# Optimization experiments

Hardware: AMD Instinct MI355X
Metric: run time of the kernel (lower is better)

Reference implementation:

```python
import jax, jax.numpy as jnp
import numpy as np

DIM = 4096
N_HEADS = 32
N_KV_HEADS = 8
HEAD_DIM = DIM // N_HEADS      # 128
N_REP = N_HEADS // N_KV_HEADS  # 4
B, S = 2, 2048
THETA = 10000.0


def _rope_tables(seq_len, head_dim):
    # standard llama2.c freqs: [1, S, 1, head_dim//2]
    freqs = 1.0 / (THETA ** (np.arange(0, head_dim, 2, dtype=np.float32) / head_dim))
    t = np.arange(seq_len, dtype=np.float32)
    ang = np.outer(t, freqs)  # [S, head_dim//2]
    cos = jnp.asarray(np.cos(ang))[None, :, None, :]
    sin = jnp.asarray(np.sin(ang))[None, :, None, :]
    return cos, sin


def setup_inputs() -> dict:
    key = jax.random.key(0)
    ks = jax.random.split(key, 5)
    x = jax.random.normal(ks[0], (B, S, DIM), dtype=jnp.float32)
    freqs_cos, freqs_sin = _rope_tables(S, HEAD_DIM)
    scale = 1.0 / np.sqrt(DIM)
    wq = jax.random.normal(ks[1], (DIM, N_HEADS * HEAD_DIM), dtype=jnp.float32) * scale
    wk = jax.random.normal(ks[2], (DIM, N_KV_HEADS * HEAD_DIM), dtype=jnp.float32) * scale
    wv = jax.random.normal(ks[3], (DIM, N_KV_HEADS * HEAD_DIM), dtype=jnp.float32) * scale
    wo = jax.random.normal(ks[4], (N_HEADS * HEAD_DIM, DIM), dtype=jnp.float32) * scale
    return {"x": x, "freqs_cos": freqs_cos, "freqs_sin": freqs_sin,
            "wq": wq, "wk": wk, "wv": wv, "wo": wo}


def _apply_rotary(t, cos, sin):
    # t: [B, S, H, head_dim]; cos/sin: [1, S, 1, head_dim//2]
    b, s, h, d = t.shape
    tr = t.reshape(b, s, h, d // 2, 2)
    t_r, t_i = tr[..., 0], tr[..., 1]
    out_r = t_r * cos - t_i * sin
    out_i = t_r * sin + t_i * cos
    return jnp.stack([out_r, out_i], axis=-1).reshape(b, s, h, d)


def reference(x, freqs_cos, freqs_sin, wq, wk, wv, wo):
    b, s, _ = x.shape
    q = (x @ wq).reshape(b, s, N_HEADS, HEAD_DIM)
    k = (x @ wk).reshape(b, s, N_KV_HEADS, HEAD_DIM)
    v = (x @ wv).reshape(b, s, N_KV_HEADS, HEAD_DIM)
    q = _apply_rotary(q, freqs_cos, freqs_sin)
    k = _apply_rotary(k, freqs_cos, freqs_sin)
    # GQA: repeat kv heads to match q heads
    k = jnp.repeat(k, N_REP, axis=2)  # [b, s, H, hd]
    v = jnp.repeat(v, N_REP, axis=2)
    # NOTE: source calls SDPA with attn_mask=None and no is_causal -> non-causal
    scores = jnp.einsum('bqhd,bkhd->bhqk', q, k) / jnp.sqrt(
        jnp.asarray(HEAD_DIM, dtype=q.dtype))
    attn = jax.nn.softmax(scores, axis=-1)
    out = jnp.einsum('bhqk,bkhd->bqhd', attn, v)
    out = out.reshape(b, s, N_HEADS * HEAD_DIM)
    return out @ wo
```

## Files before the change

kernel.cpp:

```cpp
#include <hip/hip_runtime.h>
#include <cstdint>


typedef __attribute__((ext_vector_type(8))) short short8;
typedef __attribute__((ext_vector_type(4))) float f32x4;
typedef __attribute__((ext_vector_type(16))) float f32x16;

__device__ __forceinline__ float bf2f(unsigned short u) {
  union { unsigned int i; float f; } v; v.i = ((unsigned int)u) << 16; return v.f;
}
__device__ __forceinline__ unsigned short f2bf(float f) {
  union { float f; unsigned int i; } v; v.f = f;
  unsigned int r = v.i + 0x7fffu + ((v.i >> 16) & 1u);
  return (unsigned short)(r >> 16);
}

__device__ __forceinline__ void gload_lds16(const void* g, void* lds) {
  __builtin_amdgcn_global_load_lds(
      (const __attribute__((address_space(1))) unsigned int*)g,
      (__attribute__((address_space(3))) unsigned int*)lds, 16, 0, 0);
}

__device__ __forceinline__ unsigned int cvtpk_bf16(float lo, float hi) {
  unsigned int r;
  asm("v_cvt_pk_bf16_f32 %0, %1, %2" : "=v"(r) : "v"(lo), "v"(hi));
  return r;
}
__device__ __forceinline__ void pl32swap(unsigned int& a, unsigned int& b) {
  asm("v_permlane32_swap_b32 %0, %1" : "+v"(a), "+v"(b));
}


__global__ __launch_bounds__(256) void cast_bf16(const float* __restrict__ src,
                                                 unsigned short* __restrict__ dst) {
  size_t i = (size_t)blockIdx.x * 256 + threadIdx.x;
  float4 v = ((const float4*)src)[i];
  ushort4 o; o.x = f2bf(v.x); o.y = f2bf(v.y); o.z = f2bf(v.z); o.w = f2bf(v.w);
  ((ushort4*)dst)[i] = o;
}

__global__ __launch_bounds__(256) void transpose_cast(const float* __restrict__ src,
                                                      unsigned short* __restrict__ dst,
                                                      int R, int C) {
  __shared__ float tile[32][33];
  int c0 = blockIdx.x * 32, r0 = blockIdx.y * 32;
  int tx = threadIdx.x & 31, ty = threadIdx.x >> 5;
#pragma unroll
  for (int j = 0; j < 4; ++j)
    tile[ty + j * 8][tx] = src[(size_t)(r0 + ty + j * 8) * C + c0 + tx];
  __syncthreads();
#pragma unroll
  for (int j = 0; j < 4; ++j)
    dst[(size_t)(c0 + ty + j * 8) * R + r0 + tx] = f2bf(tile[tx][ty + j * 8]);
}

__global__ __launch_bounds__(256) void rope_k(unsigned short* __restrict__ qkv,
                                              const float* __restrict__ cosT,
                                              const float* __restrict__ sinT) {
  int idx = blockIdx.x * 256 + threadIdx.x;
  int t = idx / 640;
  int cb = (idx - t * 640) * 8;
  int s = t & 2047;
  int j0 = (cb & 127) >> 1;
  unsigned short* p = qkv + (size_t)t * 6144 + cb;
  uint4 u = *(const uint4*)p;
  float4 c4 = *(const float4*)&cosT[s * 64 + j0];
  float4 s4 = *(const float4*)&sinT[s * 64 + j0];
  auto rot = [](unsigned int& uu, float c, float sn) {
    float re = bf2f((unsigned short)(uu & 0xffffu));
    float im = bf2f((unsigned short)(uu >> 16));
    float nr = re * c - im * sn;
    float ni = re * sn + im * c;
    uu = (unsigned int)f2bf(nr) | ((unsigned int)f2bf(ni) << 16);
  };
  rot(u.x, c4.x, s4.x); rot(u.y, c4.y, s4.y);
  rot(u.z, c4.z, s4.z); rot(u.w, c4.w, s4.w);
  *(uint4*)p = u;
}

__global__ __launch_bounds__(256) void transpose_v(const unsigned short* __restrict__ qkv,
                                                   unsigned short* __restrict__ vt) {
  __shared__ unsigned short tile[32][33];
  int bk = blockIdx.z;
  int s0 = blockIdx.x * 32, d0 = blockIdx.y * 32;
  int tx = threadIdx.x & 31, ty = threadIdx.x >> 5;
  int b = bk >> 3, kvh = bk & 7;
#pragma unroll
  for (int j = 0; j < 4; ++j)
    tile[ty + j * 8][tx] =
        qkv[(size_t)(b * 2048 + s0 + ty + j * 8) * 6144 + 5120 + kvh * 128 + d0 + tx];
  __syncthreads();
#pragma unroll
  for (int j = 0; j < 4; ++j)
    vt[(size_t)(bk * 128 + d0 + ty + j * 8) * 2048 + s0 + tx] = tile[tx][ty + j * 8];
}


#define GBAR() asm volatile("s_barrier" ::: "memory")
#define GVM6() asm volatile("s_waitcnt vmcnt(6)" ::: "memory")
#define GVM4() asm volatile("s_waitcnt vmcnt(4)" ::: "memory")
#define GHINT() asm volatile("s_waitcnt lgkmcnt(8)" ::: "memory")

#define GLDA(buf, mh)                                                                   \
  do {                                                                                  \
    _Pragma("unroll") for (int m_ = 0; m_ < 4; ++m_)                                    \
    _Pragma("unroll") for (int ks_ = 0; ks_ < 2; ++ks_)                                 \
      a[m_][ks_] = *(const short8*)&smem[buf][0]                                        \
          [(wm * 128 + (mh) * 64 + m_ * 16 + lr) * 64 + (((ks_ * 4 + lg) ^ (lr & 7)) << 3)]; \
  } while (0)

#define GLDB(bf_, buf, nh)                                                              \
  do {                                                                                  \
    _Pragma("unroll") for (int n_ = 0; n_ < 2; ++n_)                                    \
    _Pragma("unroll") for (int ks_ = 0; ks_ < 2; ++ks_)                                 \
      bf_[n_][ks_] = *(const short8*)&smem[buf][1]                                      \
          [(wn * 64 + (nh) * 32 + n_ * 16 + lr) * 64 + (((ks_ * 4 + lg) ^ (lr & 7)) << 3)]; \
  } while (0)

#define GMM(bf_, mh, nh)                                                                \
  do {                                                                                  \
    __builtin_amdgcn_s_setprio(1);                                                      \
    _Pragma("unroll") for (int ks_ = 0; ks_ < 2; ++ks_)                                 \
    _Pragma("unroll") for (int m_ = 0; m_ < 4; ++m_)                                    \
    _Pragma("unroll") for (int n_ = 0; n_ < 2; ++n_)                                    \
      acc[(mh) * 4 + m_][(nh) * 2 + n_] = __builtin_amdgcn_mfma_f32_16x16x32_bf16(      \
          a[m_][ks_], bf_[n_][ks_], acc[(mh) * 4 + m_][(nh) * 2 + n_], 0, 0, 0);        \
    __builtin_amdgcn_s_setprio(0);                                                      \
  } while (0)

#define GSTG(half, buf, tile)                                                           \
  do {                                                                                  \
    _Pragma("unroll") for (int t2_ = 0; t2_ < 2; ++t2_)                                 \
      gload_lds16(srcp[half][t2_] + ((size_t)(tile) << 6),                              \
                  &smem[buf][(half) >> 1][dsto[half][t2_]]);                            \
  } while (0)

template <typename OutT>
__device__ __forceinline__ void gemm256_body(const unsigned short* __restrict__ A,
                                             const unsigned short* __restrict__ B,
                                             OutT* __restrict__ C, int K, int ldc,
                                             unsigned short (*smem)[2][16384]) {
  const int bid = blockIdx.x;
  const int xcd = bid & 7, ii = bid >> 3;
  const int mt = (xcd & 3) * 4 + (ii & 3);
  const int nt = (xcd >> 2) * 8 + (ii >> 2);
  const int m0 = mt * 256, n0 = nt * 256;
  const int tid = threadIdx.x, w = tid >> 6, l = tid & 63;
  const int wm = w >> 2, wn = w & 3;
  const int lr = l & 15, lg = l >> 4;
  const int NT = K >> 6;

  const int lsub = l >> 3, lgr = l & 7;
  const int sg = (lgr ^ lsub) << 3;
  const unsigned short* srcp[4][2];
  int dsto[4][2];
#pragma unroll
  for (int t2 = 0; t2 < 2; ++t2) {
    int lb = t2 * 64 + w * 8;
    int pa0 = (lb & 63) + ((lb >> 6) << 7);
    int pb0 = (lb & 31) + ((lb >> 5) << 6);
    srcp[0][t2] = A + (size_t)(m0 + pa0 + lsub) * K + sg;       dsto[0][t2] = pa0 * 64;
    srcp[1][t2] = A + (size_t)(m0 + pa0 + 64 + lsub) * K + sg;  dsto[1][t2] = (pa0 + 64) * 64;
    srcp[2][t2] = B + (size_t)(n0 + pb0 + lsub) * K + sg;       dsto[2][t2] = pb0 * 64;
    srcp[3][t2] = B + (size_t)(n0 + pb0 + 32 + lsub) * K + sg;  dsto[3][t2] = (pb0 + 32) * 64;
  }

  f32x4 acc[8][4] = {};
  short8 a[4][2], b0f[2][2], b1f[2][2];

  GSTG(0, 0, 0); GSTG(2, 0, 0); GSTG(3, 0, 0); GSTG(1, 0, 0);
  GSTG(0, 1, 1); GSTG(2, 1, 1); GSTG(3, 1, 1);
  GVM6();
  GBAR();

  for (int t = 0; t < NT / 2; ++t) {
    const int t1 = 2 * t + 1;
    const int t2a = (2 * t + 2 < NT) ? 2 * t + 2 : NT - 1;
    const int t2b = (2 * t + 3 < NT) ? 2 * t + 3 : NT - 1;
    GLDA(0, 0); GLDB(b0f, 0, 0);
    GSTG(1, 1, t1);
    GHINT();
    GBAR(); GMM(b0f, 0, 0); GBAR();
    GLDB(b1f, 0, 1);
    GSTG(0, 0, t2a);
    GBAR(); GMM(b1f, 0, 1); GBAR();
    GLDA(0, 1);
    GSTG(2, 0, t2a);
    GBAR(); GMM(b0f, 1, 0); GBAR();
    GSTG(3, 0, t2a);
    GBAR(); GMM(b1f, 1, 1); GVM6(); GBAR();
    GLDA(1, 0); GLDB(b0f, 1, 0);
    GSTG(1, 0, t2a);
    GHINT();
    GBAR(); GMM(b0f, 0, 0); GBAR();
    GLDB(b1f, 1, 1);
    GSTG(0, 1, t2b);
    GBAR(); GMM(b1f, 0, 1); GBAR();
    GLDA(1, 1);
    GSTG(2, 1, t2b);
    GBAR(); GMM(b0f, 1, 0); GBAR();
    GSTG(3, 1, t2b);
    GBAR(); GMM(b1f, 1, 1); GVM6(); GBAR();
  }

#pragma unroll
  for (int m = 0; m < 8; ++m)
#pragma unroll
    for (int n = 0; n < 4; ++n)
#pragma unroll
      for (int r = 0; r < 4; ++r) {
        int row = m0 + wm * 128 + m * 16 + lg * 4 + r;
        int col = n0 + wn * 64 + n * 16 + lr;
        float v = acc[m][n][r];
        if constexpr (sizeof(OutT) == 2)
          C[(size_t)row * ldc + col] = (OutT)f2bf(v);
        else
          C[(size_t)row * ldc + col] = v;
      }
}

__global__ __launch_bounds__(512) void gemm_qproj(const unsigned short* __restrict__ A,
                                                  const unsigned short* __restrict__ B,
                                                  unsigned short* __restrict__ C,
                                                  int K, int ldc) {
  __shared__ unsigned short smem[2][2][16384];
  gemm256_body<unsigned short>(A, B, C, K, ldc, smem);
}

__global__ __launch_bounds__(512) void gemm_oproj(const unsigned short* __restrict__ A,
                                                  const unsigned short* __restrict__ B,
                                                  float* __restrict__ C,
                                                  int K, int ldc) {
  __shared__ unsigned short smem[2][2][16384];
  gemm256_body<float>(A, B, C, K, ldc, smem);
}


#define KLDA(buf)                                                                       \
  do {                                                                                  \
    _Pragma("unroll") for (int m_ = 0; m_ < 4; ++m_)                                    \
    _Pragma("unroll") for (int ks_ = 0; ks_ < 2; ++ks_)                                 \
      a2[m_][ks_] = *(const short8*)&As2[buf]                                           \
          [(wm * 64 + m_ * 16 + lr) * 64 + (((ks_ * 4 + lg) ^ (lr & 7)) << 3)];         \
  } while (0)

#define KLDB(bf_, buf, nh)                                                              \
  do {                                                                                  \
    _Pragma("unroll") for (int n_ = 0; n_ < 2; ++n_)                                    \
    _Pragma("unroll") for (int ks_ = 0; ks_ < 2; ++ks_)                                 \
      bf_[n_][ks_] = *(const short8*)&Bs2[buf]                                          \
          [(wn * 64 + (nh) * 32 + n_ * 16 + lr) * 64 + (((ks_ * 4 + lg) ^ (lr & 7)) << 3)]; \
  } while (0)

#define KMM(bf_, nh)                                                                    \
  do {                                                                                  \
    __builtin_amdgcn_s_setprio(1);                                                      \
    _Pragma("unroll") for (int ks_ = 0; ks_ < 2; ++ks_)                                 \
    _Pragma("unroll") for (int m_ = 0; m_ < 4; ++m_)                                    \
    _Pragma("unroll") for (int n_ = 0; n_ < 2; ++n_)                                    \
      acc[m_][(nh) * 2 + n_] = __builtin_amdgcn_mfma_f32_16x16x32_bf16(                 \
          a2[m_][ks_], bf_[n_][ks_], acc[m_][(nh) * 2 + n_], 0, 0, 0);                  \
    __builtin_amdgcn_s_setprio(0);                                                      \
  } while (0)

#define KSTGA(buf, tile)                                                                \
  do {                                                                                  \
    _Pragma("unroll") for (int t2_ = 0; t2_ < 2; ++t2_)                                 \
      gload_lds16(srcA[t2_] + ((size_t)(tile) << 6), &As2[buf][dstA[t2_]]);             \
  } while (0)
#define KSTGB0(buf, tile)                                                               \
  do {                                                                                  \
    _Pragma("unroll") for (int t2_ = 0; t2_ < 2; ++t2_)                                 \
      gload_lds16(srcB0[t2_] + ((size_t)(tile) << 6), &Bs2[buf][dstB0[t2_]]);           \
  } while (0)
#define KSTGB1(buf, tile)                                                               \
  do {                                                                                  \
    _Pragma("unroll") for (int t2_ = 0; t2_ < 2; ++t2_)                                 \
      gload_lds16(srcB1[t2_] + ((size_t)(tile) << 6), &Bs2[buf][dstB1[t2_]]);           \
  } while (0)

__global__ __launch_bounds__(512) void gemm_kvproj(const unsigned short* __restrict__ A,
                                                   const unsigned short* __restrict__ B,
                                                   unsigned short* __restrict__ C,
                                                   int K, int ldc) {
  __shared__ unsigned short As2[2][8192];
  __shared__ unsigned short Bs2[2][16384];
  const int bid = blockIdx.x;
  const int xcd = bid & 7, ii = bid >> 3;
  const int mt = (xcd & 3) * 8 + (ii & 7);
  const int nt = (xcd >> 2) * 4 + (ii >> 3);
  const int m0 = mt * 128, n0 = nt * 256;
  const int tid = threadIdx.x, w = tid >> 6, l = tid & 63;
  const int wm = w >> 2, wn = w & 3;
  const int lr = l & 15, lg = l >> 4;
  const int NT = K >> 6;

  const int lsub = l >> 3, lgr = l & 7;
  const int sg = (lgr ^ lsub) << 3;
  const unsigned short* srcA[2];  int dstA[2];
  const unsigned short* srcB0[2]; int dstB0[2];
  const unsigned short* srcB1[2]; int dstB1[2];
#pragma unroll
  for (int t2 = 0; t2 < 2; ++t2) {
    int ra = t2 * 64 + w * 8;
    srcA[t2] = A + (size_t)(m0 + ra + lsub) * K + sg;            dstA[t2] = ra * 64;
    int lb = t2 * 64 + w * 8;
    int pb0 = (lb & 31) + ((lb >> 5) << 6);
    srcB0[t2] = B + (size_t)(n0 + pb0 + lsub) * K + sg;          dstB0[t2] = pb0 * 64;
    srcB1[t2] = B + (size_t)(n0 + pb0 + 32 + lsub) * K + sg;     dstB1[t2] = (pb0 + 32) * 64;
  }

  f32x4 acc[4][4] = {};
  short8 a2[4][2], bb0[2][2], bb1[2][2];

  KSTGA(0, 0); KSTGB0(0, 0); KSTGB1(0, 0);
  KSTGA(1, 1); KSTGB0(1, 1);
  GVM4();
  GBAR();

  for (int t = 0; t < NT / 2; ++t) {
    const int t1 = 2 * t + 1;
    const int t2a = (2 * t + 2 < NT) ? 2 * t + 2 : NT - 1;
    const int t2b = (2 * t + 3 < NT) ? 2 * t + 3 : NT - 1;
    KLDA(0); KLDB(bb0, 0, 0);
    KSTGB1(1, t1);
    GHINT();
    GBAR(); KMM(bb0, 0); GBAR();
    KLDB(bb1, 0, 1);
    KSTGA(0, t2a); KSTGB0(0, t2a);
    GBAR(); KMM(bb1, 1); GVM4(); GBAR();
    KLDA(1); KLDB(bb0, 1, 0);
    KSTGB1(0, t2a);
    GHINT();
    GBAR(); KMM(bb0, 0); GBAR();
    KLDB(bb1, 1, 1);
    KSTGA(1, t2b); KSTGB0(1, t2b);
    GBAR(); KMM(bb1, 1); GVM4(); GBAR();
  }

#pragma unroll
  for (int m = 0; m < 4; ++m)
#pragma unroll
    for (int n = 0; n < 4; ++n)
#pragma unroll
      for (int r = 0; r < 4; ++r) {
        int row = m0 + wm * 64 + m * 16 + lg * 4 + r;
        int col = n0 + wn * 64 + n * 16 + lr;
        C[(size_t)row * ldc + col] = f2bf(acc[m][n][r]);
      }
}


__global__ __launch_bounds__(256, 2) void attn_k(const unsigned short* __restrict__ qkv,
                                                 const unsigned short* __restrict__ vt,
                                                 unsigned short* __restrict__ ctx) {
  __shared__ unsigned short Ks[2][64 * 128];
  __shared__ unsigned short Vs[2][128 * 64];
  const int bid = blockIdx.x;
  const int xcd = bid & 7, idx = bid >> 3;
  const int kvg = xcd * 2 + (idx >> 6);
  const int hg = (idx >> 4) & 3;
  const int qt = idx & 15;
  const int b = kvg >> 3, kvh = kvg & 7, h = kvh * 4 + hg;
  const int w = threadIdx.x >> 6, l = threadIdx.x & 63;
  const int lc = l & 31, hi = l >> 5;
  const size_t tok0 = (size_t)b * 2048;
  const int q0 = qt * 128 + w * 32;
  const float C2 = 0.12751744516557944f;
  const float THR = 4.0f / C2;

  const unsigned short* ksrc[4];
  const unsigned short* vsrc[4];
#pragma unroll
  for (int i = 0; i < 4; ++i) {
    int L = w * 256 + i * 64 + l;
    int krow = L >> 4, kc = L & 15;
    ksrc[i] = qkv + (tok0 + krow) * 6144 + 4096 + kvh * 128 + ((kc ^ (krow & 7)) << 3);
    int vrow = L >> 3, vc = L & 7;
    vsrc[i] = vt + (size_t)(kvg * 128 + vrow) * 2048 + ((vc ^ (vrow & 7)) << 3);
  }
  const int ldsBase = (w * 256) * 8;

  auto stage = [&](int bufi, int kv0s) {
#pragma unroll
    for (int i = 0; i < 4; ++i)
      gload_lds16(ksrc[i] + (size_t)kv0s * 6144, &Ks[bufi][ldsBase + i * 512]);
#pragma unroll
    for (int i = 0; i < 4; ++i)
      gload_lds16(vsrc[i] + kv0s, &Vs[bufi][ldsBase + i * 512]);
  };

  const unsigned short* Qb = qkv + (tok0 + q0 + lc) * 6144 + h * 128 + hi * 8;
  short8 qf[8];
#pragma unroll
  for (int dc = 0; dc < 8; ++dc) qf[dc] = *(const short8*)(Qb + dc * 16);

  f32x16 acc[4] = {};
  float m = -1e30f, lsum = 0.f;

  stage(0, 0);
  __syncthreads();

  int buf = 0;
  for (int kt = 0; kt < 32; ++kt) {
    if (kt < 31) stage(buf ^ 1, (kt + 1) * 64);
    const int swz = (lc & 7) << 3;
    f32x16 s0 = {}, s1 = {};
#pragma unroll
    for (int dc = 0; dc < 8; ++dc) {
      int cidx = ((dc * 2 + hi) << 3) ^ swz;
      short8 kf0 = *(const short8*)&Ks[buf][lc * 128 + cidx];
      short8 kf1 = *(const short8*)&Ks[buf][(lc + 32) * 128 + cidx];
      s0 = __builtin_amdgcn_mfma_f32_32x32x16_bf16(kf0, qf[dc], s0, 0, 0, 0);
      s1 = __builtin_amdgcn_mfma_f32_32x32x16_bf16(kf1, qf[dc], s1, 0, 0, 0);
    }
    float tm = fmaxf(s0[0], s1[0]);
#pragma unroll
    for (int r = 1; r < 16; ++r) tm = fmaxf(tm, fmaxf(s0[r], s1[r]));
    tm = fmaxf(tm, __shfl_xor(tm, 32, 64));
    if (__any(tm > m + THR)) {
      float mn = fmaxf(m, tm);
      float sc = __builtin_amdgcn_exp2f((m - mn) * C2);
      m = mn;
      lsum *= sc;
#pragma unroll
      for (int r = 0; r < 16; ++r) {
        float sr = __shfl(sc, (r & 3) + 8 * (r >> 2) + 4 * hi, 64);
#pragma unroll
        for (int dt = 0; dt < 4; ++dt) acc[dt][r] *= sr;
      }
    }
    float p[32];
    float ts = 0.f;
#pragma unroll
    for (int r = 0; r < 16; ++r) p[r] = __builtin_amdgcn_exp2f((s0[r] - m) * C2);
#pragma unroll
    for (int r = 0; r < 16; ++r) p[16 + r] = __builtin_amdgcn_exp2f((s1[r] - m) * C2);
#pragma unroll
    for (int r = 0; r < 32; ++r) ts += p[r];
    ts += __shfl_xor(ts, 32, 64);
    lsum += ts;
    short8 pa[4];
#pragma unroll
    for (int g = 0; g < 4; ++g) {
      unsigned int c0 = cvtpk_bf16(p[g * 8 + 0], p[g * 8 + 1]);
      unsigned int c1 = cvtpk_bf16(p[g * 8 + 2], p[g * 8 + 3]);
      unsigned int c2 = cvtpk_bf16(p[g * 8 + 4], p[g * 8 + 5]);
      unsigned int c3 = cvtpk_bf16(p[g * 8 + 6], p[g * 8 + 7]);
      pl32swap(c0, c2);
      pl32swap(c1, c3);
      union { unsigned int u[4]; short8 v; } t;
      t.u[0] = c0; t.u[1] = c1; t.u[2] = c2; t.u[3] = c3;
      pa[g] = t.v;
    }
#pragma unroll
    for (int dt = 0; dt < 4; ++dt) {
#pragma unroll
      for (int ks = 0; ks < 4; ++ks) {
        short8 vf = *(const short8*)&Vs[buf][(dt * 32 + lc) * 64 + ((((ks * 2 + hi) << 3) ^ swz))];
        acc[dt] = __builtin_amdgcn_mfma_f32_32x32x16_bf16(pa[ks], vf, acc[dt], 0, 0, 0);
      }
    }
    __syncthreads();
    buf ^= 1;
  }
  float rl = 1.0f / lsum;
#pragma unroll
  for (int r = 0; r < 16; ++r) {
    int crow = (r & 3) + 8 * (r >> 2) + 4 * hi;
    float rlr = __shfl(rl, crow, 64);
    unsigned short* cp = ctx + (tok0 + q0 + crow) * 4096 + h * 128 + lc;
#pragma unroll
    for (int dt = 0; dt < 4; ++dt) cp[dt * 32] = f2bf(acc[dt][r] * rlr);
  }
}


extern "C" void kernel_launch(void* const* d_in, const int* in_sizes, int n_in,
                              void* d_out, int out_size, void* d_ws, size_t ws_size,
                              hipStream_t stream) {
  const float* x  = (const float*)d_in[0];
  const float* fc = (const float*)d_in[1];
  const float* fs = (const float*)d_in[2];
  const float* wq = (const float*)d_in[3];
  const float* wk = (const float*)d_in[4];
  const float* wv = (const float*)d_in[5];
  const float* wo = (const float*)d_in[6];
  float* out = (float*)d_out;
  char* ws = (char*)d_ws;

  constexpr size_t SZ_WQKVT = (size_t)6144 * 4096 * 2;
  constexpr size_t SZ_WOT   = (size_t)4096 * 4096 * 2;
  constexpr size_t SZ_QKV   = (size_t)4096 * 6144 * 2;
  constexpr size_t SZ_VT    = (size_t)16 * 128 * 2048 * 2;

  unsigned short* wqkvT = (unsigned short*)ws;
  unsigned short* woT   = (unsigned short*)(ws + SZ_WQKVT);
  unsigned short* qkv   = (unsigned short*)(ws + SZ_WQKVT + SZ_WOT);
  unsigned short* vt    = (unsigned short*)(ws + SZ_WQKVT + SZ_WOT + SZ_QKV);
  unsigned short* xbf   = (unsigned short*)(ws + SZ_WQKVT + SZ_WOT + SZ_QKV + SZ_VT);
  unsigned short* ctx   = xbf;

  cast_bf16<<<16384, 256, 0, stream>>>(x, xbf);
  transpose_cast<<<dim3(128, 128), 256, 0, stream>>>(wq, wqkvT, 4096, 4096);
  transpose_cast<<<dim3(32, 128), 256, 0, stream>>>(wk, wqkvT + (size_t)4096 * 4096, 4096, 1024);
  transpose_cast<<<dim3(32, 128), 256, 0, stream>>>(wv, wqkvT + (size_t)5120 * 4096, 4096, 1024);
  transpose_cast<<<dim3(128, 128), 256, 0, stream>>>(wo, woT, 4096, 4096);

  gemm_qproj<<<256, 512, 0, stream>>>(xbf, wqkvT, qkv, 4096, 6144);
  gemm_kvproj<<<256, 512, 0, stream>>>(xbf, wqkvT + (size_t)4096 * 4096, qkv + 4096, 4096, 6144);
  rope_k<<<10240, 256, 0, stream>>>(qkv, fc, fs);
  transpose_v<<<dim3(64, 4, 16), 256, 0, stream>>>(qkv, vt);
  attn_k<<<1024, 256, 0, stream>>>(qkv, vt, ctx);
  gemm_oproj<<<256, 512, 0, stream>>>(ctx, woT, out, 4096, 4096);
}
```

Baseline: 526.9 us.

## Fuse RoPE into projection GEMM epilogues and shrink attention KV tile for occupancy

Removes the standalone RoPE kernel and applies the rotation in the Q and KV projection GEMM epilogues, using a lane shuffle to pair adjacent real/imag columns. This saves a full read-modify-write pass over the qkv buffer. Separately, the attention kernel processes 32 keys per step instead of 64, with K double-buffered per step and V staged every two steps. The smaller LDS footprint and fewer registers allow launch bounds of 3 blocks per CU, at the cost of more loop iterations and barriers.

Result: slower. 564.1 us (+7.1%).

```diff
diff --git a/kernel.cpp b/kernel.cpp
--- a/kernel.cpp
+++ b/kernel.cpp
@@ -52,30 +52,6 @@
 #pragma unroll
   for (int j = 0; j < 4; ++j)
     dst[(size_t)(c0 + ty + j * 8) * R + r0 + tx] = f2bf(tile[tx][ty + j * 8]);
-}
-
-__global__ __launch_bounds__(256) void rope_k(unsigned short* __restrict__ qkv,
-                                              const float* __restrict__ cosT,
-                                              const float* __restrict__ sinT) {
-  int idx = blockIdx.x * 256 + threadIdx.x;
-  int t = idx / 640;
-  int cb = (idx - t * 640) * 8;
-  int s = t & 2047;
-  int j0 = (cb & 127) >> 1;
-  unsigned short* p = qkv + (size_t)t * 6144 + cb;
-  uint4 u = *(const uint4*)p;
-  float4 c4 = *(const float4*)&cosT[s * 64 + j0];
-  float4 s4 = *(const float4*)&sinT[s * 64 + j0];
-  auto rot = [](unsigned int& uu, float c, float sn) {
-    float re = bf2f((unsigned short)(uu & 0xffffu));
-    float im = bf2f((unsigned short)(uu >> 16));
-    float nr = re * c - im * sn;
-    float ni = re * sn + im * c;
-    uu = (unsigned int)f2bf(nr) | ((unsigned int)f2bf(ni) << 16);
-  };
-  rot(u.x, c4.x, s4.x); rot(u.y, c4.y, s4.y);
-  rot(u.z, c4.z, s4.z); rot(u.w, c4.w, s4.w);
-  *(uint4*)p = u;
 }
 
 __global__ __launch_bounds__(256) void transpose_v(const unsigned short* __restrict__ qkv,
@@ -135,10 +111,12 @@
                   &smem[buf][(half) >> 1][dsto[half][t2_]]);                            \
   } while (0)
 
-template <typename OutT>
+template <int ROPE, typename OutT>
 __device__ __forceinline__ void gemm256_body(const unsigned short* __restrict__ A,
                                              const unsigned short* __restrict__ B,
                                              OutT* __restrict__ C, int K, int ldc,
+                                             const float* __restrict__ fc,
+                                             const float* __restrict__ fs,
                                              unsigned short (*smem)[2][16384]) {
   const int bid = blockIdx.x;
   const int xcd = bid & 7, ii = bid >> 3;
@@ -206,25 +184,35 @@
 #pragma unroll
   for (int m = 0; m < 8; ++m)
 #pragma unroll
-    for (int n = 0; n < 4; ++n)
+    for (int n = 0; n < 4; ++n) {
+      const int col = n0 + wn * 64 + n * 16 + lr;
+      const int j = (col & 127) >> 1;
 #pragma unroll
       for (int r = 0; r < 4; ++r) {
         int row = m0 + wm * 128 + m * 16 + lg * 4 + r;
-        int col = n0 + wn * 64 + n * 16 + lr;
         float v = acc[m][n][r];
+        if constexpr (ROPE == 1) {
+          float pv = __shfl_xor(v, 1, 64);
+          int srow = row & 2047;
+          float cc = fc[srow * 64 + j], ss = fs[srow * 64 + j];
+          v = (lr & 1) ? (pv * ss + v * cc) : (v * cc - pv * ss);
+        }
         if constexpr (sizeof(OutT) == 2)
           C[(size_t)row * ldc + col] = (OutT)f2bf(v);
         else
           C[(size_t)row * ldc + col] = v;
       }
+    }
 }
 
 __global__ __launch_bounds__(512) void gemm_qproj(const unsigned short* __restrict__ A,
                                                   const unsigned short* __restrict__ B,
                                                   unsigned short* __restrict__ C,
-                                                  int K, int ldc) {
+                                                  int K, int ldc,
+                                                  const float* __restrict__ fc,
+                                                  const float* __restrict__ fs) {
   __shared__ unsigned short smem[2][2][16384];
-  gemm256_body<unsigned short>(A, B, C, K, ldc, smem);
+  gemm256_body<1, unsigned short>(A, B, C, K, ldc, fc, fs, smem);
 }
 
 __global__ __launch_bounds__(512) void gemm_oproj(const unsigned short* __restrict__ A,
@@ -232,7 +220,7 @@
                                                   float* __restrict__ C,
                                                   int K, int ldc) {
   __shared__ unsigned short smem[2][2][16384];
-  gemm256_body<float>(A, B, C, K, ldc, smem);
+  gemm256_body<0, float>(A, B, C, K, ldc, nullptr, nullptr, smem);
 }
 
 
@@ -282,7 +270,9 @@
 __global__ __launch_bounds__(512) void gemm_kvproj(const unsigned short* __restrict__ A,
                                                    const unsigned short* __restrict__ B,
                                                    unsigned short* __restrict__ C,
-                                                   int K, int ldc) {
+                                                   int K, int ldc,
+                                                   const float* __restrict__ fc,
+                                                   const float* __restrict__ fs) {
   __shared__ unsigned short As2[2][8192];
   __shared__ unsigned short Bs2[2][16384];
   const int bid = blockIdx.x;
@@ -341,20 +331,30 @@
 #pragma unroll
   for (int m = 0; m < 4; ++m)
 #pragma unroll
-    for (int n = 0; n < 4; ++n)
+    for (int n = 0; n < 4; ++n) {
+      const int col = n0 + wn * 64 + n * 16 + lr;
+      const int j = (col & 127) >> 1;
+      const bool doRope = col < 1024;
 #pragma unroll
       for (int r = 0; r < 4; ++r) {
         int row = m0 + wm * 64 + m * 16 + lg * 4 + r;
-        int col = n0 + wn * 64 + n * 16 + lr;
-        C[(size_t)row * ldc + col] = f2bf(acc[m][n][r]);
+        float v = acc[m][n][r];
+        if (doRope) {
+          float pv = __shfl_xor(v, 1, 64);
+          int srow = row & 2047;
+          float cc = fc[srow * 64 + j], ss = fs[srow * 64 + j];
+          v = (lr & 1) ? (pv * ss + v * cc) : (v * cc - pv * ss);
+        }
+        C[(size_t)row * ldc + col] = f2bf(v);
       }
-}
-
-
-__global__ __launch_bounds__(256, 2) void attn_k(const unsigned short* __restrict__ qkv,
+    }
+}
+
+
+__global__ __launch_bounds__(256, 3) void attn_k(const unsigned short* __restrict__ qkv,
                                                  const unsigned short* __restrict__ vt,
                                                  unsigned short* __restrict__ ctx) {
-  __shared__ unsigned short Ks[2][64 * 128];
+  __shared__ unsigned short Ks[2][32 * 128];
   __shared__ unsigned short Vs[2][128 * 64];
   const int bid = blockIdx.x;
   const int xcd = bid & 7, idx = bid >> 3;
@@ -369,25 +369,30 @@
   const float C2 = 0.12751744516557944f;
   const float THR = 4.0f / C2;
 
-  const unsigned short* ksrc[4];
+  const unsigned short* ksrc[2];
   const unsigned short* vsrc[4];
+#pragma unroll
+  for (int i = 0; i < 2; ++i) {
+    int L = w * 128 + i * 64 + l;
+    int krow = L >> 4, kc = L & 15;
+    ksrc[i] = qkv + (tok0 + krow) * 6144 + 4096 + kvh * 128 + ((kc ^ (krow & 7)) << 3);
+  }
 #pragma unroll
   for (int i = 0; i < 4; ++i) {
     int L = w * 256 + i * 64 + l;
-    int krow = L >> 4, kc = L & 15;
-    ksrc[i] = qkv + (tok0 + krow) * 6144 + 4096 + kvh * 128 + ((kc ^ (krow & 7)) << 3);
     int vrow = L >> 3, vc = L & 7;
     vsrc[i] = vt + (size_t)(kvg * 128 + vrow) * 2048 + ((vc ^ (vrow & 7)) << 3);
   }
-  const int ldsBase = (w * 256) * 8;
-
-  auto stage = [&](int bufi, int kv0s) {
+
+  auto stageK = [&](int bufi, int kt2) {
+#pragma unroll
+    for (int i = 0; i < 2; ++i)
+      gload_lds16(ksrc[i] + (size_t)kt2 * 32 * 6144, &Ks[bufi][w * 1024 + i * 512]);
+  };
+  auto stageV = [&](int bufi, int kv0) {
 #pragma unroll
     for (int i = 0; i < 4; ++i)
-      gload_lds16(ksrc[i] + (size_t)kv0s * 6144, &Ks[bufi][ldsBase + i * 512]);
-#pragma unroll
-    for (int i = 0; i < 4; ++i)
-      gload_lds16(vsrc[i] + kv0s, &Vs[bufi][ldsBase + i * 512]);
+      gload_lds16(vsrc[i] + kv0, &Vs[bufi][w * 2048 + i * 512]);
   };
 
   const unsigned short* Qb = qkv + (tok0 + q0 + lc) * 6144 + h * 128 + hi * 8;
@@ -398,25 +403,25 @@
   f32x16 acc[4] = {};
   float m = -1e30f, lsum = 0.f;
 
-  stage(0, 0);
+  stageK(0, 0);
+  stageV(0, 0);
   __syncthreads();
 
-  int buf = 0;
-  for (int kt = 0; kt < 32; ++kt) {
-    if (kt < 31) stage(buf ^ 1, (kt + 1) * 64);
-    const int swz = (lc & 7) << 3;
-    f32x16 s0 = {}, s1 = {};
+  const int swz = (lc & 7) << 3;
+  for (int kt = 0; kt < 64; ++kt) {
+    const int Kb = kt & 1, Vb = (kt >> 1) & 1;
+    if (kt + 1 < 64) stageK(Kb ^ 1, kt + 1);
+    if (!(kt & 1) && kt + 2 < 64) stageV(Vb ^ 1, (kt + 2) * 32);
+    f32x16 s0 = {};
 #pragma unroll
     for (int dc = 0; dc < 8; ++dc) {
       int cidx = ((dc * 2 + hi) << 3) ^ swz;
-      short8 kf0 = *(const short8*)&Ks[buf][lc * 128 + cidx];
-      short8 kf1 = *(const short8*)&Ks[buf][(lc + 32) * 128 + cidx];
+      short8 kf0 = *(const short8*)&Ks[Kb][lc * 128 + cidx];
       s0 = __builtin_amdgcn_mfma_f32_32x32x16_bf16(kf0, qf[dc], s0, 0, 0, 0);
-      s1 = __builtin_amdgcn_mfma_f32_32x32x16_bf16(kf1, qf[dc], s1, 0, 0, 0);
     }
-    float tm = fmaxf(s0[0], s1[0]);
-#pragma unroll
-    for (int r = 1; r < 16; ++r) tm = fmaxf(tm, fmaxf(s0[r], s1[r]));
+    float tm = s0[0];
+#pragma unroll
+    for (int r = 1; r < 16; ++r) tm = fmaxf(tm, s0[r]);
     tm = fmaxf(tm, __shfl_xor(tm, 32, 64));
     if (__any(tm > m + THR)) {
       float mn = fmaxf(m, tm);
@@ -430,19 +435,15 @@
         for (int dt = 0; dt < 4; ++dt) acc[dt][r] *= sr;
       }
     }
-    float p[32];
+    float p[16];
     float ts = 0.f;
 #pragma unroll
-    for (int r = 0; r < 16; ++r) p[r] = __builtin_amdgcn_exp2f((s0[r] - m) * C2);
-#pragma unroll
-    for (int r = 0; r < 16; ++r) p[16 + r] = __builtin_amdgcn_exp2f((s1[r] - m) * C2);
-#pragma unroll
-    for (int r = 0; r < 32; ++r) ts += p[r];
+    for (int r = 0; r < 16; ++r) { p[r] = __builtin_amdgcn_exp2f((s0[r] - m) * C2); ts += p[r]; }
     ts += __shfl_xor(ts, 32, 64);
     lsum += ts;
-    short8 pa[4];
-#pragma unroll
-    for (int g = 0; g < 4; ++g) {
+    short8 pa[2];
+#pragma unroll
+    for (int g = 0; g < 2; ++g) {
       unsigned int c0 = cvtpk_bf16(p[g * 8 + 0], p[g * 8 + 1]);
       unsigned int c1 = cvtpk_bf16(p[g * 8 + 2], p[g * 8 + 3]);
       unsigned int c2 = cvtpk_bf16(p[g * 8 + 4], p[g * 8 + 5]);
@@ -456,13 +457,13 @@
 #pragma unroll
     for (int dt = 0; dt < 4; ++dt) {
 #pragma unroll
-      for (int ks = 0; ks < 4; ++ks) {
-        short8 vf = *(const short8*)&Vs[buf][(dt * 32 + lc) * 64 + ((((ks * 2 + hi) << 3) ^ swz))];
-        acc[dt] = __builtin_amdgcn_mfma_f32_32x32x16_bf16(pa[ks], vf, acc[dt], 0, 0, 0);
+      for (int g = 0; g < 2; ++g) {
+        int gidx = (((kt & 1) * 4 + g * 2 + hi) << 3) ^ swz;
+        short8 vf = *(const short8*)&Vs[Vb][(dt * 32 + lc) * 64 + gidx];
+        acc[dt] = __builtin_amdgcn_mfma_f32_32x32x16_bf16(pa[g], vf, acc[dt], 0, 0, 0);
       }
     }
     __syncthreads();
-    buf ^= 1;
   }
   float rl = 1.0f / lsum;
 #pragma unroll
@@ -507,9 +508,8 @@
   transpose_cast<<<dim3(32, 128), 256, 0, stream>>>(wv, wqkvT + (size_t)5120 * 4096, 4096, 1024);
   transpose_cast<<<dim3(128, 128), 256, 0, stream>>>(wo, woT, 4096, 4096);
 
-  gemm_qproj<<<256, 512, 0, stream>>>(xbf, wqkvT, qkv, 4096, 6144);
-  gemm_kvproj<<<256, 512, 0, stream>>>(xbf, wqkvT + (size_t)4096 * 4096, qkv + 4096, 4096, 6144);
-  rope_k<<<10240, 256, 0, stream>>>(qkv, fc, fs);
+  gemm_qproj<<<256, 512, 0, stream>>>(xbf, wqkvT, qkv, 4096, 6144, fc, fs);
+  gemm_kvproj<<<256, 512, 0, stream>>>(xbf, wqkvT + (size_t)4096 * 4096, qkv + 4096, 4096, 6144, fc, fs);
   transpose_v<<<dim3(64, 4, 16), 256, 0, stream>>>(qkv, vt);
   attn_k<<<1024, 256, 0, stream>>>(qkv, vt, ctx);
   gemm_oproj<<<256, 512, 0, stream>>>(ctx, woT, out, 4096, 4096);
```
